# Kernel tuning notes

Measured on AMD Instinct MI355X. Metric: run time of the kernel, lower is better.

The kernel has to match this reference:

```python
import jax, jax.numpy as jnp
import numpy as np

N_ITER = 2
BIG = 1e16  # distance assigned to out-of-range superpixel neighbors (zero affinity)


def reference(x, stoken_size):
    B, C, H, W = x.shape
    sh = sw = int(stoken_size)
    nh, nw = H // sh, W // sw
    ns = nh * nw          # num_spixels
    P = H * W             # n_pixel

    pix = x.reshape(B, C, P)  # (B,C,P)
    # initial centroids: adaptive_avg_pool2d == block mean for divisible sizes
    spix = x.reshape(B, C, nh, sh, nw, sw).mean(axis=(3, 5)).reshape(B, C, ns)

    # init label map (nearest interpolation of the ns-label grid to HxW)
    ly = jnp.arange(H) // sh
    lx = jnp.arange(W) // sw
    init_label = (ly[:, None] * nw + lx[None, :]).reshape(-1)  # (P,)

    # 9-neighbor relative superpixel offsets
    rel = jnp.array([-nw - 1, -nw, -nw + 1, -1, 0, 1, nw - 1, nw, nw + 1])
    sidx = init_label[None, :] + rel[:, None]          # (9,P)
    valid = (sidx >= 0) & (sidx < ns)                  # same mask as get_abs_indices
    sidx_c = jnp.clip(sidx, 0, ns - 1)                 # safe gather index
    cols = jnp.broadcast_to(jnp.arange(P)[None, :], (9, P))
    bidx = jnp.broadcast_to(sidx_c[None], (B, 9, P))

    pn = (pix ** 2).sum(axis=1)   # (B,P)
    abs_aff = jnp.zeros((B, ns, P), x.dtype)
    for k in range(N_ITER):
        # pairwise squared distance pixel <-> 9 candidate superpixels
        sn = (spix ** 2).sum(axis=1)                        # (B,ns)
        dots = jnp.einsum('bcs,bcp->bsp', spix, pix)        # (B,ns,P)
        cross = jnp.take_along_axis(dots, bidx, axis=1)     # (B,9,P)
        sng = sn[:, sidx_c]                                 # (B,9,P)
        dist = pn[:, None, :] - 2.0 * cross + sng           # (B,9,P)
        dist = jnp.where(valid[None], dist, jnp.asarray(BIG, x.dtype))
        aff = jax.nn.softmax(-dist, axis=1) * valid[None]   # (B,9,P)
        # dense sparse-scatter: abs_aff[b, sidx[k,p], p] += aff[b,k,p]
        abs_aff = jnp.zeros((B, ns, P), x.dtype).at[:, sidx_c, cols].add(aff)
        if k < N_ITER - 1:
            num = jnp.einsum('bsp,bcp->bcs', abs_aff, pix)             # (B,C,ns)
            spix = num / (abs_aff.sum(axis=2)[:, None, :] + 1e-16)
    # entire ssn_iter runs under torch.no_grad in the original
    return (jax.lax.stop_gradient(abs_aff), ns)


def setup_inputs() -> dict:
    key = jax.random.key(0)
    x = jax.random.normal(key, (4, 64, 256, 256), dtype=jnp.float32)
    return {"x": x, "stoken_size": 16}
```

## Files before the change

### kernel.cpp

```cpp
#include <hip/hip_runtime.h>

#define BB 4
#define CCH 64
#define HH 256
#define WW 256
#define PP (HH*WW)
#define NS 256
#define NW 16


__global__ __launch_bounds__(256) void kA_spix_init(const float* __restrict__ x,
                                                    float* __restrict__ spix) {
    int blk = blockIdx.x;
    int i = blk & 15;
    int c = (blk >> 4) & 63;
    int b = blk >> 10;
    int t = threadIdx.x;
    const float* base = x + ((size_t)(b*CCH + c))*PP + (size_t)i*16*WW + t;
    float s = 0.f;
    #pragma unroll
    for (int r = 0; r < 16; ++r) s += base[(size_t)r*WW];
    #pragma unroll
    for (int off = 8; off; off >>= 1) s += __shfl_down(s, off, 16);
    if ((t & 15) == 0) {
        int j = t >> 4;
        spix[((size_t)b*NS + (i*16 + j))*CCH + c] = s * (1.f/256.f);
    }
}

__global__ __launch_bounds__(256) void kB_aff(const float* __restrict__ x,
                                              const float* __restrict__ spix,
                                              float* __restrict__ aff9) {
    __shared__ float spw[50][65];
    __shared__ float snw[50];
    int blk = blockIdx.x;
    int y = blk & 255;
    int b = blk >> 8;
    int t = threadIdx.x;
    int ly = y >> 4;
    int base = ly*16 - 17;

    for (int idx = t; idx < 50*CCH; idx += 256) {
        int j = idx >> 6, c = idx & 63;
        int g = base + j;
        float v = 0.f;
        if (g >= 0 && g < NS) v = spix[((size_t)b*NS + g)*CCH + c];
        spw[j][c] = v;
    }
    __syncthreads();
    if (t < 50) {
        float s = 0.f;
        #pragma unroll 8
        for (int c = 0; c < CCH; ++c) { float v = spw[t][c]; s += v*v; }
        snw[t] = s;
    }
    __syncthreads();

    int p = y*WW + t;
    const float* px = x + (size_t)b*CCH*PP + p;
    int wl = 17 + (t >> 4);
    int nk[9];
    #pragma unroll
    for (int k = 0; k < 9; ++k) nk[k] = wl + (k/3 - 1)*16 + (k%3 - 1);

    float cross[9];
    #pragma unroll
    for (int k = 0; k < 9; ++k) cross[k] = 0.f;
    float pn = 0.f;
    for (int c = 0; c < CCH; ++c) {
        float v = px[(size_t)c*PP];
        pn += v*v;
        #pragma unroll
        for (int k = 0; k < 9; ++k) cross[k] += spw[nk[k]][c] * v;
    }

    int label = ly*16 + (t >> 4);
    float e[9];
    float m = -1e30f;
    #pragma unroll
    for (int k = 0; k < 9; ++k) {
        int rel = (k/3 - 1)*16 + (k%3 - 1);
        int sidx = label + rel;
        bool valid = (sidx >= 0) && (sidx < NS);
        float z = -(pn - 2.f*cross[k] + snw[nk[k]]);
        e[k] = valid ? z : -3.0e38f;
        if (valid && z > m) m = z;
    }
    float sum = 0.f;
    #pragma unroll
    for (int k = 0; k < 9; ++k) {
        float v = (e[k] > -2.9e38f) ? expf(e[k] - m) : 0.f;
        e[k] = v;
        sum += v;
    }
    float inv = 1.f / sum;
    #pragma unroll
    for (int k = 0; k < 9; ++k)
        aff9[((size_t)b*9 + k)*PP + p] = e[k] * inv;
}

__global__ __launch_bounds__(256) void kC_partial(const float* __restrict__ x,
                                                  const float* __restrict__ aff9,
                                                  float* __restrict__ partial,
                                                  float* __restrict__ wpart) {
    __shared__ float pixT[32][257];
    __shared__ float affL[9][260];
    __shared__ float red[8][9][33];
    int blk = blockIdx.x;
    int l = blk & 255, b = blk >> 8;
    int by = l >> 4, bx = l & 15;
    int t = threadIdx.x;
    int gp = (by*16 + (t >> 4))*WW + bx*16 + (t & 15);

    #pragma unroll
    for (int k = 0; k < 9; ++k)
        affL[k][t] = aff9[((size_t)b*9 + k)*PP + gp];
    __syncthreads();

    int cl = t & 31, q = t >> 5;
    for (int half = 0; half < 2; ++half) {
        #pragma unroll 4
        for (int ci = 0; ci < 32; ++ci)
            pixT[ci][t] = x[((size_t)(b*CCH + half*32 + ci))*PP + gp];
        __syncthreads();
        float acc[9];
        #pragma unroll
        for (int k = 0; k < 9; ++k) acc[k] = 0.f;
        for (int i = 0; i < 32; ++i) {
            int lp = q*32 + i;
            float v = pixT[cl][lp];
            #pragma unroll
            for (int k = 0; k < 9; ++k) acc[k] += affL[k][lp] * v;
        }
        #pragma unroll
        for (int k = 0; k < 9; ++k) red[q][k][cl] = acc[k];
        __syncthreads();
        for (int tt = t; tt < 9*32; tt += 256) {
            int k = tt >> 5, c2 = tt & 31;
            float s = 0.f;
            #pragma unroll
            for (int qq = 0; qq < 8; ++qq) s += red[qq][k][c2];
            partial[(((size_t)b*9 + k)*NS + l)*CCH + half*32 + c2] = s;
        }
        __syncthreads();
    }
    if (t < 72) {
        int k = t >> 3, seg = t & 7;
        float s = 0.f;
        #pragma unroll
        for (int i = 0; i < 32; ++i) s += affL[k][seg*32 + i];
        red[seg][k][32] = s;
    }
    __syncthreads();
    if (t < 9) {
        float s = 0.f;
        #pragma unroll
        for (int qq = 0; qq < 8; ++qq) s += red[qq][t][32];
        wpart[((size_t)b*9 + t)*NS + l] = s;
    }
}

__global__ __launch_bounds__(256) void kD_update(const float* __restrict__ partial,
                                                 const float* __restrict__ wpart,
                                                 float* __restrict__ spix) {
    int gid = blockIdx.x*256 + threadIdx.x;
    int c = gid & 63, s = (gid >> 6) & 255, b = gid >> 14;
    float num = 0.f, den = 0.f;
    #pragma unroll
    for (int k = 0; k < 9; ++k) {
        int rel = (k/3 - 1)*16 + (k%3 - 1);
        int l = s - rel;
        if (l >= 0 && l < NS) {
            num += partial[(((size_t)b*9 + k)*NS + l)*CCH + c];
            den += wpart[((size_t)b*9 + k)*NS + l];
        }
    }
    spix[((size_t)b*NS + s)*CCH + c] = num / (den + 1e-16f);
}

__global__ __launch_bounds__(256) void kE_out(const float* __restrict__ aff9,
                                              float* __restrict__ out,
                                              int out_size) {
    int gid = blockIdx.x*256 + threadIdx.x;
    int row = gid >> 14;
    int col4 = gid & 16383;
    int s = row & 255, b = row >> 8;
    int p = col4 << 2;
    int l = ((p >> 12) << 4) | ((p & 255) >> 4);
    int diff = s - l + 17;
    float4 v = make_float4(0.f, 0.f, 0.f, 0.f);
    if ((unsigned)diff <= 34u && (diff & 15) < 3) {
        int k = (diff >> 4)*3 + (diff & 15);
        const float4* src = (const float4*)(aff9 + ((size_t)b*9 + k)*PP);
        v = src[col4];
    }
    ((float4*)out)[gid] = v;
    if (gid == 0) out[out_size - 1] = 256.0f;
}

extern "C" void kernel_launch(void* const* d_in, const int* in_sizes, int n_in,
                              void* d_out, int out_size, void* d_ws, size_t ws_size,
                              hipStream_t stream) {
    (void)in_sizes; (void)n_in; (void)ws_size;
    const float* x = (const float*)d_in[0];
    float* out = (float*)d_out;
    float* ws = (float*)d_ws;

    float* spix    = ws;
    float* aff9    = spix + (size_t)BB*NS*CCH;
    float* partial = aff9 + (size_t)BB*9*PP;
    float* wpart   = partial + (size_t)BB*9*NS*CCH;

    kA_spix_init<<<BB*CCH*16, 256, 0, stream>>>(x, spix);
    kB_aff<<<BB*HH, 256, 0, stream>>>(x, spix, aff9);
    kC_partial<<<BB*NS, 256, 0, stream>>>(x, aff9, partial, wpart);
    kD_update<<<BB*NS*CCH/256, 256, 0, stream>>>(partial, wpart, spix);
    kB_aff<<<BB*HH, 256, 0, stream>>>(x, spix, aff9);
    kE_out<<<(BB*NS*PP/4)/256, 256, 0, stream>>>(aff9, out, out_size);
}
```

Before: 126.6 us.

## Fuse first-iteration affinity computation with partial centroid accumulation per superpixel block

Replaces the first kB_aff launch and kC_partial with a single kernel that computes the 9-neighbor softmax affinities for each 16x16 superpixel block in shared memory and immediately accumulates the per-block partial centroid sums. This avoids writing and re-reading the 9xP affinity map for iteration one and removes a kernel launch. The reduction buffer now aliases the pixel tile, which needs an extra barrier, and x is read twice within the kernel with strided per-channel loads.

```diff
diff --git a/kernel.cpp b/kernel.cpp
--- a/kernel.cpp
+++ b/kernel.cpp
@@ -25,6 +25,120 @@
     if ((t & 15) == 0) {
         int j = t >> 4;
         spix[((size_t)b*NS + (i*16 + j))*CCH + c] = s * (1.f/256.f);
+    }
+}
+
+__global__ __launch_bounds__(256) void kF_fused(const float* __restrict__ x,
+                                                const float* __restrict__ spix,
+                                                float* __restrict__ partial,
+                                                float* __restrict__ wpart) {
+    __shared__ float sp[9][64];
+    __shared__ float sn[9];
+    __shared__ float affL[9][260];
+    __shared__ float pixT[32][257];
+    float (*red)[9][33] = (float(*)[9][33])&pixT[0][0];
+
+    int blk = blockIdx.x;
+    int l = blk & 255, b = blk >> 8;
+    int by = l >> 4, bx = l & 15;
+    int t = threadIdx.x;
+
+    for (int idx = t; idx < 9*64; idx += 256) {
+        int k = idx >> 6, c = idx & 63;
+        int rel = (k/3 - 1)*16 + (k % 3) - 1;
+        int s = l + rel;
+        float v = 0.f;
+        if (s >= 0 && s < NS) v = spix[((size_t)b*NS + s)*CCH + c];
+        sp[k][c] = v;
+    }
+    __syncthreads();
+    if (t < 9) {
+        float s = 0.f;
+        #pragma unroll 8
+        for (int c = 0; c < CCH; ++c) { float v = sp[t][c]; s += v*v; }
+        sn[t] = s;
+    }
+    __syncthreads();
+
+    int ty = t >> 4, tx = t & 15;
+    int gp = (by*16 + ty)*WW + bx*16 + tx;
+    const float* px = x + (size_t)b*CCH*PP + gp;
+
+    float cross[9];
+    #pragma unroll
+    for (int k = 0; k < 9; ++k) cross[k] = 0.f;
+    float pn = 0.f;
+    for (int c = 0; c < CCH; ++c) {
+        float v = px[(size_t)c*PP];
+        pn += v*v;
+        #pragma unroll
+        for (int k = 0; k < 9; ++k) cross[k] += sp[k][c] * v;
+    }
+
+    float e[9];
+    float m = -1e30f;
+    #pragma unroll
+    for (int k = 0; k < 9; ++k) {
+        int rel = (k/3 - 1)*16 + (k % 3) - 1;
+        int s = l + rel;
+        bool valid = (s >= 0) && (s < NS);
+        float z = -(pn - 2.f*cross[k] + sn[k]);
+        e[k] = valid ? z : -3.0e38f;
+        if (valid && z > m) m = z;
+    }
+    float sum = 0.f;
+    #pragma unroll
+    for (int k = 0; k < 9; ++k) {
+        float v = (e[k] > -2.9e38f) ? expf(e[k] - m) : 0.f;
+        e[k] = v;
+        sum += v;
+    }
+    float inv = 1.f / sum;
+    #pragma unroll
+    for (int k = 0; k < 9; ++k) affL[k][t] = e[k] * inv;
+    __syncthreads();
+
+    int cl = t & 31, q = t >> 5;
+    for (int half = 0; half < 2; ++half) {
+        #pragma unroll 4
+        for (int ci = 0; ci < 32; ++ci)
+            pixT[ci][t] = x[((size_t)(b*CCH + half*32 + ci))*PP + gp];
+        __syncthreads();
+        float acc[9];
+        #pragma unroll
+        for (int k = 0; k < 9; ++k) acc[k] = 0.f;
+        for (int i = 0; i < 32; ++i) {
+            int lp = q*32 + i;
+            float v = pixT[cl][lp];
+            #pragma unroll
+            for (int k = 0; k < 9; ++k) acc[k] += affL[k][lp] * v;
+        }
+        __syncthreads();
+        #pragma unroll
+        for (int k = 0; k < 9; ++k) red[q][k][cl] = acc[k];
+        __syncthreads();
+        for (int tt = t; tt < 9*32; tt += 256) {
+            int k = tt >> 5, c2 = tt & 31;
+            float s = 0.f;
+            #pragma unroll
+            for (int qq = 0; qq < 8; ++qq) s += red[qq][k][c2];
+            partial[(((size_t)b*9 + k)*NS + l)*CCH + half*32 + c2] = s;
+        }
+        __syncthreads();
+    }
+    if (t < 72) {
+        int k = t >> 3, seg = t & 7;
+        float s = 0.f;
+        #pragma unroll
+        for (int i = 0; i < 32; ++i) s += affL[k][seg*32 + i];
+        red[seg][k][32] = s;
+    }
+    __syncthreads();
+    if (t < 9) {
+        float s = 0.f;
+        #pragma unroll
+        for (int qq = 0; qq < 8; ++qq) s += red[qq][t][32];
+        wpart[((size_t)b*9 + t)*NS + l] = s;
     }
 }
 
@@ -97,67 +211,6 @@
     #pragma unroll
     for (int k = 0; k < 9; ++k)
         aff9[((size_t)b*9 + k)*PP + p] = e[k] * inv;
-}
-
-__global__ __launch_bounds__(256) void kC_partial(const float* __restrict__ x,
-                                                  const float* __restrict__ aff9,
-                                                  float* __restrict__ partial,
-                                                  float* __restrict__ wpart) {
-    __shared__ float pixT[32][257];
-    __shared__ float affL[9][260];
-    __shared__ float red[8][9][33];
-    int blk = blockIdx.x;
-    int l = blk & 255, b = blk >> 8;
-    int by = l >> 4, bx = l & 15;
-    int t = threadIdx.x;
-    int gp = (by*16 + (t >> 4))*WW + bx*16 + (t & 15);
-
-    #pragma unroll
-    for (int k = 0; k < 9; ++k)
-        affL[k][t] = aff9[((size_t)b*9 + k)*PP + gp];
-    __syncthreads();
-
-    int cl = t & 31, q = t >> 5;
-    for (int half = 0; half < 2; ++half) {
-        #pragma unroll 4
-        for (int ci = 0; ci < 32; ++ci)
-            pixT[ci][t] = x[((size_t)(b*CCH + half*32 + ci))*PP + gp];
-        __syncthreads();
-        float acc[9];
-        #pragma unroll
-        for (int k = 0; k < 9; ++k) acc[k] = 0.f;
-        for (int i = 0; i < 32; ++i) {
-            int lp = q*32 + i;
-            float v = pixT[cl][lp];
-            #pragma unroll
-            for (int k = 0; k < 9; ++k) acc[k] += affL[k][lp] * v;
-        }
-        #pragma unroll
-        for (int k = 0; k < 9; ++k) red[q][k][cl] = acc[k];
-        __syncthreads();
-        for (int tt = t; tt < 9*32; tt += 256) {
-            int k = tt >> 5, c2 = tt & 31;
-            float s = 0.f;
-            #pragma unroll
-            for (int qq = 0; qq < 8; ++qq) s += red[qq][k][c2];
-            partial[(((size_t)b*9 + k)*NS + l)*CCH + half*32 + c2] = s;
-        }
-        __syncthreads();
-    }
-    if (t < 72) {
-        int k = t >> 3, seg = t & 7;
-        float s = 0.f;
-        #pragma unroll
-        for (int i = 0; i < 32; ++i) s += affL[k][seg*32 + i];
-        red[seg][k][32] = s;
-    }
-    __syncthreads();
-    if (t < 9) {
-        float s = 0.f;
-        #pragma unroll
-        for (int qq = 0; qq < 8; ++qq) s += red[qq][t][32];
-        wpart[((size_t)b*9 + t)*NS + l] = s;
-    }
 }
 
 __global__ __launch_bounds__(256) void kD_update(const float* __restrict__ partial,
@@ -212,8 +265,7 @@
     float* wpart   = partial + (size_t)BB*9*NS*CCH;
 
     kA_spix_init<<<BB*CCH*16, 256, 0, stream>>>(x, spix);
-    kB_aff<<<BB*HH, 256, 0, stream>>>(x, spix, aff9);
-    kC_partial<<<BB*NS, 256, 0, stream>>>(x, aff9, partial, wpart);
+    kF_fused<<<BB*NS, 256, 0, stream>>>(x, spix, partial, wpart);
     kD_update<<<BB*NS*CCH/256, 256, 0, stream>>>(partial, wpart, spix);
     kB_aff<<<BB*HH, 256, 0, stream>>>(x, spix, aff9);
     kE_out<<<(BB*NS*PP/4)/256, 256, 0, stream>>>(aff9, out, out_size);
```

New measurement: 127.6 us. Within noise of the previous version (+0.8%).
